# Optimization experiments

Measured on AMD Instinct MI355X. Metric: run time of the kernel, lower is better.

Reference implementation:

```python
import jax, jax.numpy as jnp
import numpy as np
from jax import lax


def _conv(x, w, padding):
    # NCHW input, OIHW weights, stride 1, no bias
    return lax.conv_general_dilated(x, w, (1, 1), padding,
                                    dimension_numbers=('NCHW', 'OIHW', 'NCHW'))


def setup_inputs() -> dict:
    key = jax.random.key(0)
    ks = jax.random.split(key, 6)
    B, C, H, W = 16, 512, 40, 40
    return {
        'exemplar': jax.random.normal(ks[0], (B, C, H, W), jnp.float32),
        'query':    jax.random.normal(ks[1], (B, C, H, W), jnp.float32),
        'w_e':  jax.random.normal(ks[2], (256, C, 1, 1), jnp.float32) * 0.01,
        'w_q':  jax.random.normal(ks[3], (256, C, 1, 1), jnp.float32) * 0.01,
        'w_c1': jax.random.normal(ks[4], (C, C, 3, 3), jnp.float32) * 0.01,
        'w_c2': jax.random.normal(ks[5], (C, C, 3, 3), jnp.float32) * 0.01,
    }


def reference(exemplar, query, w_e, w_q, w_c1, w_c2):
    B, C, H, W = query.shape
    N = H * W
    # 1x1 projections to 256-dim correlation space
    q_corr = _conv(query, w_q, 'VALID').reshape(B, -1, N)     # [B,256,N]
    e_corr = _conv(exemplar, w_e, 'VALID').reshape(B, -1, N)  # [B,256,N]
    # A[b, n_exemplar, m_query] = <e_corr[:, n], q_corr[:, m]>
    A = jnp.einsum('bcn,bcm->bnm', e_corr, q_corr)            # [B,N,N]
    # A1 = softmax over exemplar axis, then transpose (torch: softmax(A,dim=1).T)
    A1 = jnp.swapaxes(jax.nn.softmax(A, axis=1), 1, 2)        # [B,N,N]
    # Bm = softmax(A^T, dim=1).T  == softmax(A, axis=2)
    Bm = jnp.swapaxes(jax.nn.softmax(jnp.swapaxes(A, 1, 2), axis=1), 1, 2)
    e_flat = exemplar.reshape(B, C, N)
    q_flat = query.reshape(B, C, N)
    query_att = jnp.matmul(e_flat, A1)   # [B,C,N]
    exemplar_att = jnp.matmul(q_flat, Bm)  # [B,C,N]
    input1_att = _conv(exemplar_att.reshape(B, C, H, W), w_c1, 'SAME')
    input2_att = _conv(query_att.reshape(B, C, H, W), w_c2, 'SAME')
    return jnp.concatenate([input1_att, input2_att], axis=1)  # [B,2C,H,W]
```

## Files before the change

### kernel.cpp

```cpp
#include <hip/hip_runtime.h>

typedef unsigned short u16;
typedef __attribute__((ext_vector_type(8))) short bf16x8;
typedef __attribute__((ext_vector_type(4))) float f32x4;

__device__ __forceinline__ u16 f2bf(float f) {
  union { float f; unsigned u; } v; v.f = f;
  unsigned u = v.u;
  u += 0x7fffu + ((u >> 16) & 1u);
  return (u16)(u >> 16);
}

__device__ __forceinline__ void gll16(const void* g, void* l) {
  __builtin_amdgcn_global_load_lds(
      (const __attribute__((address_space(1))) void*)g,
      (__attribute__((address_space(3))) void*)l, 16, 0, 0);
}

__global__ __launch_bounds__(256) void transp_cast_x2(const float* __restrict__ ex,
                                                      const float* __restrict__ qu,
                                                      u16* __restrict__ xte,
                                                      u16* __restrict__ xtq) {
  __shared__ float t[32][33];
  int z = blockIdx.z;
  int b = z & 15;
  const float* xb = (z < 16 ? ex : qu) + (size_t)b * 819200;
  u16* xtb = (z < 16 ? xte : xtq) + (size_t)b * 819200;
  int n0 = blockIdx.x * 32, c0 = blockIdx.y * 32;
  int tx = threadIdx.x & 31, ty = threadIdx.x >> 5;
#pragma unroll
  for (int k = 0; k < 4; k++) {
    int c = ty + k * 8;
    t[c][tx] = xb[(size_t)(c0 + c) * 1600 + n0 + tx];
  }
  __syncthreads();
#pragma unroll
  for (int k = 0; k < 4; k++) {
    int n = ty + k * 8;
    xtb[(size_t)(n0 + n) * 512 + c0 + tx] = f2bf(t[tx][n]);
  }
}

__global__ void cast_w(const float* __restrict__ we, const float* __restrict__ wq,
                       u16* __restrict__ oe, u16* __restrict__ oq) {
  int i = blockIdx.x * 256 + threadIdx.x;
  oe[i] = f2bf(we[i]);
  oq[i] = f2bf(wq[i]);
}

__global__ void repack_wc(const float* __restrict__ w1, const float* __restrict__ w2,
                          u16* __restrict__ o1, u16* __restrict__ o2) {
  const float* w = blockIdx.y ? w2 : w1;
  u16* wr = blockIdx.y ? o2 : o1;
  int idx = blockIdx.x * 256 + threadIdx.x;
  int o = idx / 4608;
  int r = idx - o * 4608;
  int t = r >> 9;
  int c = r & 511;
  wr[idx] = f2bf(w[o * 4608 + c * 9 + t]);
}

__global__ void zero_mem(uint4* __restrict__ p, long n) {
  long i = (long)blockIdx.x * blockDim.x + threadIdx.x;
  long stride = (long)gridDim.x * blockDim.x;
  uint4 z; z.x = 0; z.y = 0; z.z = 0; z.w = 0;
  for (; i < n; i += stride) p[i] = z;
}

template <int MODE>
__global__ __launch_bounds__(256) void gemm_bt64(
    const u16* __restrict__ A, const u16* __restrict__ B, u16* __restrict__ C,
    const u16* __restrict__ A2, const u16* __restrict__ B2, u16* __restrict__ C2,
    int M, int N, int K, long sA, long sB, long sC) {
  __shared__ u16 lds_a[128 * 64];
  __shared__ u16 lds_b[128 * 64];
  int tid = threadIdx.x;
  int z = blockIdx.z, b = z & 15;
  const u16* Ab = (z < 16 ? A : A2) + (size_t)b * sA;
  const u16* Bb = (z < 16 ? B : B2) + (size_t)b * sB;
  u16* Cb = (z < 16 ? C : C2) + (size_t)b * sC;
  int m0 = blockIdx.x * 128, n0 = blockIdx.y * 128;

  int rsub = tid >> 3;
  int gch = (tid & 7) ^ (rsub & 7);
  long Kb = (long)K * 2;
  const char* pa[4];
  const char* pb[4];
#pragma unroll
  for (int c = 0; c < 4; c++) {
    int ra = m0 + 32 * c + rsub; ra = ra < M ? ra : M - 1;
    int rb = n0 + 32 * c + rsub; rb = rb < N ? rb : N - 1;
    pa[c] = (const char*)Ab + (long)ra * Kb + gch * 16;
    pb[c] = (const char*)Bb + (long)rb * Kb + gch * 16;
  }

  const f32x4 fzero = {0.f, 0.f, 0.f, 0.f};
  f32x4 acc[4][4];
#pragma unroll
  for (int mi = 0; mi < 4; mi++)
#pragma unroll
    for (int ni = 0; ni < 4; ni++) acc[mi][ni] = fzero;

  int wid = tid >> 6, lane = tid & 63;
  int wm = wid & 1, wn = wid >> 1;
  int lrow = lane & 15, lquad = lane >> 4;
  int sl = lrow & 7;

  int ksteps = K >> 6;
  for (int ks = 0; ks < ksteps; ks++) {
#pragma unroll
    for (int c = 0; c < 4; c++) {
      gll16(pa[c], (char*)lds_a + c * 4096 + tid * 16);
      gll16(pb[c], (char*)lds_b + c * 4096 + tid * 16);
      pa[c] += 128; pb[c] += 128;
    }
    __syncthreads();
#pragma unroll
    for (int k2 = 0; k2 < 2; k2++) {
      int sel = ((k2 << 2) | lquad) ^ sl;
      bf16x8 bv[4];
#pragma unroll
      for (int ni = 0; ni < 4; ni++) {
        int rowb = wn * 64 + ni * 16 + lrow;
        bv[ni] = *(const bf16x8*)((const char*)lds_b + rowb * 128 + sel * 16);
      }
#pragma unroll
      for (int mi = 0; mi < 4; mi++) {
        int rowa = wm * 64 + mi * 16 + lrow;
        bf16x8 av = *(const bf16x8*)((const char*)lds_a + rowa * 128 + sel * 16);
#pragma unroll
        for (int ni = 0; ni < 4; ni++)
          acc[mi][ni] =
              __builtin_amdgcn_mfma_f32_16x16x32_bf16(av, bv[ni], acc[mi][ni], 0, 0, 0);
      }
    }
    __syncthreads();
  }

#pragma unroll
  for (int mi = 0; mi < 4; mi++) {
#pragma unroll
    for (int r = 0; r < 4; r++) {
      int i = m0 + wm * 64 + mi * 16 + lquad * 4 + r;
      if (i >= M) continue;
#pragma unroll
      for (int ni = 0; ni < 4; ni++) {
        int j = n0 + wn * 64 + ni * 16 + lrow;
        if (j >= N) continue;
        float v = acc[mi][ni][r];
        if (MODE == 2) {
          int y = i / 40, x = i - y * 40;
          Cb[(size_t)((y + 1) * 42 + (x + 1)) * 512 + j] = f2bf(v);
        } else {
          Cb[(size_t)i * N + j] = f2bf(v);
        }
      }
    }
  }
}

__global__ __launch_bounds__(256) void gemm_corr_exp(
    const u16* __restrict__ A, const u16* __restrict__ B, u16* __restrict__ E,
    u16* __restrict__ ET, float* __restrict__ Zrow, float* __restrict__ Zcol) {
  __shared__ u16 lds_a[128 * 64];
  __shared__ u16 lds_b[128 * 64];
  int tid = threadIdx.x;
  int b = blockIdx.z;
  const u16* Ab = A + (size_t)b * 409600;
  const u16* Bb = B + (size_t)b * 409600;
  u16* Eb = E + (size_t)b * 2560000;
  u16* ETb = ET + (size_t)b * 2560000;
  int m0 = blockIdx.x * 128, n0 = blockIdx.y * 128;

  int rsub = tid >> 3;
  int gch = (tid & 7) ^ (rsub & 7);
  const char* pa[4];
  const char* pb[4];
#pragma unroll
  for (int c = 0; c < 4; c++) {
    int ra = m0 + 32 * c + rsub; ra = ra < 1600 ? ra : 1599;
    int rb = n0 + 32 * c + rsub; rb = rb < 1600 ? rb : 1599;
    pa[c] = (const char*)(Ab + (size_t)ra * 256) + gch * 16;
    pb[c] = (const char*)(Bb + (size_t)rb * 256) + gch * 16;
  }

  const f32x4 fzero = {0.f, 0.f, 0.f, 0.f};
  f32x4 acc[4][4];
#pragma unroll
  for (int mi = 0; mi < 4; mi++)
#pragma unroll
    for (int ni = 0; ni < 4; ni++) acc[mi][ni] = fzero;

  int wid = tid >> 6, lane = tid & 63;
  int wm = wid & 1, wn = wid >> 1;
  int lrow = lane & 15, lquad = lane >> 4;
  int sl = lrow & 7;

  for (int ks = 0; ks < 4; ks++) {
#pragma unroll
    for (int c = 0; c < 4; c++) {
      gll16(pa[c], (char*)lds_a + c * 4096 + tid * 16);
      gll16(pb[c], (char*)lds_b + c * 4096 + tid * 16);
      pa[c] += 128; pb[c] += 128;
    }
    __syncthreads();
#pragma unroll
    for (int k2 = 0; k2 < 2; k2++) {
      int sel = ((k2 << 2) | lquad) ^ sl;
      bf16x8 bv[4];
#pragma unroll
      for (int ni = 0; ni < 4; ni++) {
        int rowb = wn * 64 + ni * 16 + lrow;
        bv[ni] = *(const bf16x8*)((const char*)lds_b + rowb * 128 + sel * 16);
      }
#pragma unroll
      for (int mi = 0; mi < 4; mi++) {
        int rowa = wm * 64 + mi * 16 + lrow;
        bf16x8 av = *(const bf16x8*)((const char*)lds_a + rowa * 128 + sel * 16);
#pragma unroll
        for (int ni = 0; ni < 4; ni++)
          acc[mi][ni] =
              __builtin_amdgcn_mfma_f32_16x16x32_bf16(av, bv[ni], acc[mi][ni], 0, 0, 0);
      }
    }
    __syncthreads();
  }

  const int TS = 136;
  u16* T = lds_a;
  float colacc[4] = {0.f, 0.f, 0.f, 0.f};
#pragma unroll
  for (int s = 0; s < 4; s++) {
    if (wm == (s >> 1)) {
      int smi0 = (s & 1) * 2;
#pragma unroll
      for (int mi2 = 0; mi2 < 2; mi2++) {
        int mi = smi0 + mi2;
        float rowp[4] = {0.f, 0.f, 0.f, 0.f};
#pragma unroll
        for (int ni = 0; ni < 4; ni++) {
          int j = n0 + wn * 64 + ni * 16 + lrow;
          bool jv = j < 1600;
#pragma unroll
          for (int r = 0; r < 4; r++) {
            int i = m0 + wm * 64 + mi * 16 + lquad * 4 + r;
            float e = __expf(acc[mi][ni][r]);
            T[(mi2 * 16 + lquad * 4 + r) * TS + wn * 64 + ni * 16 + lrow] = f2bf(e);
            rowp[r] += jv ? e : 0.f;
            colacc[ni] += (i < 1600) ? e : 0.f;
          }
        }
#pragma unroll
        for (int r = 0; r < 4; r++) {
          float v = rowp[r];
          v += __shfl_xor(v, 1);
          v += __shfl_xor(v, 2);
          v += __shfl_xor(v, 4);
          v += __shfl_xor(v, 8);
          int i = m0 + wm * 64 + mi * 16 + lquad * 4 + r;
          if (lrow == 0 && i < 1600) atomicAdd(&Zrow[b * 1600 + i], v);
        }
      }
    }
    __syncthreads();
#pragma unroll
    for (int p = 0; p < 2; p++) {
      int jj = tid + p * 256;
      int ml = jj >> 4, n8 = jj & 15;
      int gi = m0 + s * 32 + ml, gj = n0 + n8 * 8;
      if (gi < 1600 && gj < 1600)
        *(uint4*)(Eb + (size_t)gi * 1600 + gj) = *(const uint4*)&T[ml * TS + n8 * 8];
    }
#pragma unroll
    for (int p = 0; p < 4; p++) {
      int jj = tid + p * 256;
      int n = jj >> 3, m4 = jj & 7;
      int gm = m0 + s * 32 + m4 * 4, gn = n0 + n;
      if (gn < 1600 && gm < 1600) {
        ushort4 v;
        v.x = T[(m4 * 4 + 0) * TS + n];
        v.y = T[(m4 * 4 + 1) * TS + n];
        v.z = T[(m4 * 4 + 2) * TS + n];
        v.w = T[(m4 * 4 + 3) * TS + n];
        *(ushort4*)(ETb + (size_t)gn * 1600 + gm) = v;
      }
    }
    __syncthreads();
  }
#pragma unroll
  for (int ni = 0; ni < 4; ni++) {
    float v = colacc[ni];
    v += __shfl_xor(v, 16);
    v += __shfl_xor(v, 32);
    int j = n0 + wn * 64 + ni * 16 + lrow;
    if (lquad == 0 && j < 1600) atomicAdd(&Zcol[b * 1600 + j], v);
  }
}

__global__ void scale_div(const float* __restrict__ ex, const float* __restrict__ qu,
                          const float* __restrict__ Zcol, const float* __restrict__ Zrow,
                          u16* __restrict__ ebf, u16* __restrict__ qbf) {
  const float* x; const float* Z; u16* o;
  if (blockIdx.y == 0) { x = ex; Z = Zcol; o = ebf; }
  else { x = qu; Z = Zrow; o = qbf; }
  size_t idx = (size_t)blockIdx.x * 256 + threadIdx.x;
  int b = (int)(idx / 819200);
  int i = (int)(idx % 1600);
  o[idx] = f2bf(x[idx] / Z[b * 1600 + i]);
}

__global__ __launch_bounds__(512, 2) void conv_gemm8p(
    const u16* __restrict__ W1, const u16* __restrict__ ATT1,
    const u16* __restrict__ W2, const u16* __restrict__ ATT2,
    float* __restrict__ out) {
  __shared__ u16 ldsA[32768];
  __shared__ u16 ldsB[32768];
  int tid = threadIdx.x;
  int z = blockIdx.z, b = z & 15, sel2 = z >> 4;
  const u16* W = sel2 ? W2 : W1;
  const u16* attb = (sel2 ? ATT2 : ATT1) + (size_t)b * 903168;
  float* outb = out + (size_t)b * 1638400 + (size_t)(sel2 ? 512 : 0) * 1600;
  int p0 = blockIdx.x * 256, o0 = blockIdx.y * 256;

  int rl = tid >> 2;
  int cs = (tid & 3) ^ ((rl >> 1) & 3);
  const char* pA0 = (const char*)(W + (size_t)(o0 + rl) * 4608) + cs * 16;
  const char* pA1 = pA0 + 128 * 9216;
  int pp0 = p0 + rl; pp0 = pp0 < 1600 ? pp0 : 1599;
  int y0 = pp0 / 40, x0 = pp0 - y0 * 40;
  const char* pB0 = (const char*)(attb + (size_t)(y0 * 42 + x0) * 512) + cs * 16;
  int pp1 = p0 + 128 + rl; pp1 = pp1 < 1600 ? pp1 : 1599;
  int y1 = pp1 / 40, x1 = pp1 - y1 * 40;
  const char* pB1 = (const char*)(attb + (size_t)(y1 * 42 + x1) * 512) + cs * 16;

  char* ldsAb = (char*)ldsA;
  char* ldsBb = (char*)ldsB;
  int dstT = tid * 16;

#define STAGE_A(d, kh, kt)                                              \
  {                                                                     \
    int ko = (kt) * 128 + (kh) * 64;                                    \
    gll16(pA0 + ko, ldsAb + ((d) * 2 + (kh)) * 16384 + dstT);           \
    gll16(pA1 + ko, ldsAb + ((d) * 2 + (kh)) * 16384 + 8192 + dstT);    \
  }
#define STAGE_B(d, kh, kt)                                              \
  {                                                                     \
    int tp = (kt) >> 3;                                                 \
    int ty = (tp * 11) >> 5;                                            \
    int tx = tp - ty * 3;                                               \
    int ko = (ty * 42 + tx) * 1024 + ((kt) & 7) * 128 + (kh) * 64;      \
    gll16(pB0 + ko, ldsBb + ((d) * 2 + (kh)) * 16384 + dstT);           \
    gll16(pB1 + ko, ldsBb + ((d) * 2 + (kh)) * 16384 + 8192 + dstT);    \
  }

  int wid = tid >> 6, lane = tid & 63;
  int wm = wid & 1, wn = wid >> 1;
  int lrow = lane & 15, lquad = lane >> 4;
  int csel = (lquad ^ ((lrow >> 1) & 3)) << 4;
  int aBase = (wm * 128 + lrow) * 64 + csel;
  int bBase = (wn * 64 + lrow) * 64 + csel;

  const f32x4 fzero = {0.f, 0.f, 0.f, 0.f};
  f32x4 acc[8][4];
#pragma unroll
  for (int mi = 0; mi < 8; mi++)
#pragma unroll
    for (int ni = 0; ni < 4; ni++) acc[mi][ni] = fzero;

  STAGE_B(0, 0, 0); STAGE_A(0, 0, 0); STAGE_B(0, 1, 0); STAGE_A(0, 1, 0);
  STAGE_B(1, 0, 1); STAGE_A(1, 0, 1); STAGE_B(1, 1, 1);
  asm volatile("s_waitcnt vmcnt(6)" ::: "memory");
  __builtin_amdgcn_s_barrier();

  bf16x8 bv0, bv1, bv2, bv3;

#define MFMA4(mi, av)                                                          \
  acc[mi][0] = __builtin_amdgcn_mfma_f32_16x16x32_bf16(av, bv0, acc[mi][0], 0, 0, 0); \
  acc[mi][1] = __builtin_amdgcn_mfma_f32_16x16x32_bf16(av, bv1, acc[mi][1], 0, 0, 0); \
  acc[mi][2] = __builtin_amdgcn_mfma_f32_16x16x32_bf16(av, bv2, acc[mi][2], 0, 0, 0); \
  acc[mi][3] = __builtin_amdgcn_mfma_f32_16x16x32_bf16(av, bv3, acc[mi][3], 0, 0, 0);

#define PHASE(d, kh, mh, STG, VM)                                              \
  {                                                                            \
    const char* ra_ = ldsAb + ((d) * 2 + (kh)) * 16384 + aBase + (mh) * 4096;  \
    bf16x8 av0 = *(const bf16x8*)(ra_);                                        \
    bf16x8 av1 = *(const bf16x8*)(ra_ + 1024);                                 \
    bf16x8 av2 = *(const bf16x8*)(ra_ + 2048);                                 \
    bf16x8 av3 = *(const bf16x8*)(ra_ + 3072);                                 \
    if ((mh) == 0) {                                                           \
      const char* rb_ = ldsBb + ((d) * 2 + (kh)) * 16384 + bBase;              \
      bv0 = *(const bf16x8*)(rb_);                                             \
      bv1 = *(const bf16x8*)(rb_ + 1024);                                      \
      bv2 = *(const bf16x8*)(rb_ + 2048);                                      \
      bv3 = *(const bf16x8*)(rb_ + 3072);                                      \
    }                                                                          \
    STG;                                                                       \
    VM;                                                                        \
    __builtin_amdgcn_s_barrier();                                              \
    asm volatile("s_waitcnt lgkmcnt(0)" ::: "memory");                         \
    __builtin_amdgcn_sched_barrier(0);                                         \
    __builtin_amdgcn_s_setprio(1);                                             \
    MFMA4((mh) * 4 + 0, av0);                                                  \
    MFMA4((mh) * 4 + 1, av1);                                                  \
    MFMA4((mh) * 4 + 2, av2);                                                  \
    MFMA4((mh) * 4 + 3, av3);                                                  \
    __builtin_amdgcn_s_setprio(0);                                             \
    __builtin_amdgcn_sched_barrier(0);                                         \
    __builtin_amdgcn_s_barrier();                                              \
  }

#define VMW asm volatile("s_waitcnt vmcnt(6)" ::: "memory")

#pragma unroll 1
  for (int it = 0; it < 36; ++it) {
    int ktb = it * 2;
    int kt1 = ktb + 1;
    int kt2 = ktb + 2 < 72 ? ktb + 2 : 71;
    int kt3 = ktb + 3 < 72 ? ktb + 3 : 71;
    PHASE(0, 0, 0, STAGE_A(1, 1, kt1), (void)0);
    PHASE(0, 0, 1, STAGE_B(0, 0, kt2), (void)0);
    PHASE(0, 1, 0, STAGE_A(0, 0, kt2), (void)0);
    PHASE(0, 1, 1, STAGE_B(0, 1, kt2), VMW);
    PHASE(1, 0, 0, STAGE_A(0, 1, kt2), (void)0);
    PHASE(1, 0, 1, STAGE_B(1, 0, kt3), (void)0);
    PHASE(1, 1, 0, STAGE_A(1, 0, kt3), (void)0);
    PHASE(1, 1, 1, STAGE_B(1, 1, kt3), VMW);
  }

#undef PHASE
#undef MFMA4
#undef VMW
#undef STAGE_A
#undef STAGE_B

#pragma unroll
  for (int mi = 0; mi < 8; mi++) {
#pragma unroll
    for (int r = 0; r < 4; r++) {
      int o = o0 + wm * 128 + mi * 16 + lquad * 4 + r;
      float* orow = outb + (size_t)o * 1600;
#pragma unroll
      for (int ni = 0; ni < 4; ni++) {
        int p = p0 + wn * 64 + ni * 16 + lrow;
        if (p < 1600) orow[p] = acc[mi][ni][r];
      }
    }
  }
}

extern "C" void kernel_launch(void* const* d_in, const int* in_sizes, int n_in,
                              void* d_out, int out_size, void* d_ws, size_t ws_size,
                              hipStream_t stream) {
  const float* ex = (const float*)d_in[0];
  const float* qu = (const float*)d_in[1];
  const float* w_e = (const float*)d_in[2];
  const float* w_q = (const float*)d_in[3];
  const float* w_c1 = (const float*)d_in[4];
  const float* w_c2 = (const float*)d_in[5];
  float* out = (float*)d_out;
  char* ws = (char*)d_ws;

  u16* E     = (u16*)(ws + 0L);
  u16* ET    = (u16*)(ws + 81920000L);
  u16* xt_e  = (u16*)(ws + 163840000L);
  u16* xt_q  = (u16*)(ws + 190054400L);
  u16* ecorr = (u16*)(ws + 216268800L);
  u16* qcorr = (u16*)(ws + 229376000L);
  u16* att_e = (u16*)(ws + 242483200L);
  u16* att_q = (u16*)(ws + 271384576L);
  float* Zrow = (float*)(ws + 300285952L);
  float* Zcol = (float*)(ws + 300388352L);
  u16* w_ebf = (u16*)(ws + 300490752L);
  u16* w_qbf = (u16*)(ws + 300752896L);
  u16* wr1   = (u16*)(ws + 301015040L);
  u16* wr2   = (u16*)(ws + 305733632L);

  transp_cast_x2<<<dim3(50, 16, 32), 256, 0, stream>>>(ex, qu, xt_e, xt_q);
  cast_w<<<dim3(512), 256, 0, stream>>>(w_e, w_q, w_ebf, w_qbf);
  repack_wc<<<dim3(9216, 2), 256, 0, stream>>>(w_c1, w_c2, wr1, wr2);
  zero_mem<<<dim3(2048), 256, 0, stream>>>((uint4*)att_e, 3625472L);

  gemm_bt64<0><<<dim3(13, 2, 32), 256, 0, stream>>>(
      xt_e, w_ebf, ecorr, xt_q, w_qbf, qcorr, 1600, 256, 512, 819200L, 0L, 409600L);

  gemm_corr_exp<<<dim3(13, 13, 16), 256, 0, stream>>>(ecorr, qcorr, E, ET, Zrow, Zcol);

  u16* ebf = xt_e;
  u16* qbf = xt_q;
  scale_div<<<dim3(51200, 2), 256, 0, stream>>>(ex, qu, Zcol, Zrow, ebf, qbf);

  gemm_bt64<2><<<dim3(13, 4, 32), 256, 0, stream>>>(
      E, ebf, att_q, ET, qbf, att_e, 1600, 512, 1600, 2560000L, 819200L, 903168L);

  conv_gemm8p<<<dim3(7, 2, 32), 512, 0, stream>>>(wr1, att_e, wr2, att_q, out);
}
```

Before: 867.0 us.

## Retile 3x3 conv GEMM to 256x224 tiles with 4x2 warp grid

Changes the conv GEMM output tile from 256x256 to 256x224 pixels, which grows the grid from 7 to 8 blocks along the pixel dimension. Each wave now computes a 64x112 sub-tile (4x7 MFMA fragments) instead of 128x64, under a 4x2 wave layout. The pipeline is restructured from eight half-phases per iteration to four full phases, each staging both A and B and waiting at vmcnt(8). The aim is to fill more CU slots and cut barrier count. The B staging still loads 256 rows, so some loads fetch unused data.

```diff
diff --git a/kernel.cpp b/kernel.cpp
--- a/kernel.cpp
+++ b/kernel.cpp
@@ -309,7 +309,7 @@
   o[idx] = f2bf(x[idx] / Z[b * 1600 + i]);
 }
 
-__global__ __launch_bounds__(512, 2) void conv_gemm8p(
+__global__ __launch_bounds__(512, 2) void conv_gemm4p(
     const u16* __restrict__ W1, const u16* __restrict__ ATT1,
     const u16* __restrict__ W2, const u16* __restrict__ ATT2,
     float* __restrict__ out) {
@@ -320,7 +320,7 @@
   const u16* W = sel2 ? W2 : W1;
   const u16* attb = (sel2 ? ATT2 : ATT1) + (size_t)b * 903168;
   float* outb = out + (size_t)b * 1638400 + (size_t)(sel2 ? 512 : 0) * 1600;
-  int p0 = blockIdx.x * 256, o0 = blockIdx.y * 256;
+  int p0 = blockIdx.x * 224, o0 = blockIdx.y * 256;
 
   int rl = tid >> 2;
   int cs = (tid & 3) ^ ((rl >> 1) & 3);
@@ -352,64 +352,66 @@
     gll16(pB0 + ko, ldsBb + ((d) * 2 + (kh)) * 16384 + dstT);           \
     gll16(pB1 + ko, ldsBb + ((d) * 2 + (kh)) * 16384 + 8192 + dstT);    \
   }
+#define STAGE_U(d, kh, kt) { STAGE_A(d, kh, kt); STAGE_B(d, kh, kt); }
 
   int wid = tid >> 6, lane = tid & 63;
-  int wm = wid & 1, wn = wid >> 1;
+  int wm = wid & 3, wn = wid >> 2;
   int lrow = lane & 15, lquad = lane >> 4;
   int csel = (lquad ^ ((lrow >> 1) & 3)) << 4;
-  int aBase = (wm * 128 + lrow) * 64 + csel;
-  int bBase = (wn * 64 + lrow) * 64 + csel;
+  int aBase = (wm * 64 + lrow) * 64 + csel;
+  int bBase = (wn * 112 + lrow) * 64 + csel;
 
   const f32x4 fzero = {0.f, 0.f, 0.f, 0.f};
-  f32x4 acc[8][4];
-#pragma unroll
-  for (int mi = 0; mi < 8; mi++)
-#pragma unroll
-    for (int ni = 0; ni < 4; ni++) acc[mi][ni] = fzero;
-
-  STAGE_B(0, 0, 0); STAGE_A(0, 0, 0); STAGE_B(0, 1, 0); STAGE_A(0, 1, 0);
-  STAGE_B(1, 0, 1); STAGE_A(1, 0, 1); STAGE_B(1, 1, 1);
-  asm volatile("s_waitcnt vmcnt(6)" ::: "memory");
+  f32x4 acc[4][7];
+#pragma unroll
+  for (int mi = 0; mi < 4; mi++)
+#pragma unroll
+    for (int ni = 0; ni < 7; ni++) acc[mi][ni] = fzero;
+
+  STAGE_U(0, 0, 0);
+  STAGE_U(0, 1, 0);
+  STAGE_U(1, 0, 1);
+  asm volatile("s_waitcnt vmcnt(8)" ::: "memory");
   __builtin_amdgcn_s_barrier();
 
-  bf16x8 bv0, bv1, bv2, bv3;
-
-#define MFMA4(mi, av)                                                          \
-  acc[mi][0] = __builtin_amdgcn_mfma_f32_16x16x32_bf16(av, bv0, acc[mi][0], 0, 0, 0); \
-  acc[mi][1] = __builtin_amdgcn_mfma_f32_16x16x32_bf16(av, bv1, acc[mi][1], 0, 0, 0); \
-  acc[mi][2] = __builtin_amdgcn_mfma_f32_16x16x32_bf16(av, bv2, acc[mi][2], 0, 0, 0); \
-  acc[mi][3] = __builtin_amdgcn_mfma_f32_16x16x32_bf16(av, bv3, acc[mi][3], 0, 0, 0);
-
-#define PHASE(d, kh, mh, STG, VM)                                              \
+#define MROW(mi, av)                                                                   \
+  acc[mi][0] = __builtin_amdgcn_mfma_f32_16x16x32_bf16(av, bv0, acc[mi][0], 0, 0, 0);  \
+  acc[mi][1] = __builtin_amdgcn_mfma_f32_16x16x32_bf16(av, bv1, acc[mi][1], 0, 0, 0);  \
+  acc[mi][2] = __builtin_amdgcn_mfma_f32_16x16x32_bf16(av, bv2, acc[mi][2], 0, 0, 0);  \
+  acc[mi][3] = __builtin_amdgcn_mfma_f32_16x16x32_bf16(av, bv3, acc[mi][3], 0, 0, 0);  \
+  acc[mi][4] = __builtin_amdgcn_mfma_f32_16x16x32_bf16(av, bv4, acc[mi][4], 0, 0, 0);  \
+  acc[mi][5] = __builtin_amdgcn_mfma_f32_16x16x32_bf16(av, bv5, acc[mi][5], 0, 0, 0);  \
+  acc[mi][6] = __builtin_amdgcn_mfma_f32_16x16x32_bf16(av, bv6, acc[mi][6], 0, 0, 0);
+
+#define PHASE(d, kh, STG)                                                      \
   {                                                                            \
-    const char* ra_ = ldsAb + ((d) * 2 + (kh)) * 16384 + aBase + (mh) * 4096;  \
+    const char* ra_ = ldsAb + ((d) * 2 + (kh)) * 16384 + aBase;                \
+    const char* rb_ = ldsBb + ((d) * 2 + (kh)) * 16384 + bBase;                \
     bf16x8 av0 = *(const bf16x8*)(ra_);                                        \
     bf16x8 av1 = *(const bf16x8*)(ra_ + 1024);                                 \
     bf16x8 av2 = *(const bf16x8*)(ra_ + 2048);                                 \
     bf16x8 av3 = *(const bf16x8*)(ra_ + 3072);                                 \
-    if ((mh) == 0) {                                                           \
-      const char* rb_ = ldsBb + ((d) * 2 + (kh)) * 16384 + bBase;              \
-      bv0 = *(const bf16x8*)(rb_);                                             \
-      bv1 = *(const bf16x8*)(rb_ + 1024);                                      \
-      bv2 = *(const bf16x8*)(rb_ + 2048);                                      \
-      bv3 = *(const bf16x8*)(rb_ + 3072);                                      \
-    }                                                                          \
+    bf16x8 bv0 = *(const bf16x8*)(rb_);                                        \
+    bf16x8 bv1 = *(const bf16x8*)(rb_ + 1024);                                 \
+    bf16x8 bv2 = *(const bf16x8*)(rb_ + 2048);                                 \
+    bf16x8 bv3 = *(const bf16x8*)(rb_ + 3072);                                 \
+    bf16x8 bv4 = *(const bf16x8*)(rb_ + 4096);                                 \
+    bf16x8 bv5 = *(const bf16x8*)(rb_ + 5120);                                 \
+    bf16x8 bv6 = *(const bf16x8*)(rb_ + 6144);                                 \
     STG;                                                                       \
-    VM;                                                                        \
+    asm volatile("s_waitcnt vmcnt(8)" ::: "memory");                           \
     __builtin_amdgcn_s_barrier();                                              \
     asm volatile("s_waitcnt lgkmcnt(0)" ::: "memory");                         \
     __builtin_amdgcn_sched_barrier(0);                                         \
     __builtin_amdgcn_s_setprio(1);                                             \
-    MFMA4((mh) * 4 + 0, av0);                                                  \
-    MFMA4((mh) * 4 + 1, av1);                                                  \
-    MFMA4((mh) * 4 + 2, av2);                                                  \
-    MFMA4((mh) * 4 + 3, av3);                                                  \
+    MROW(0, av0)                                                               \
+    MROW(1, av1)                                                               \
+    MROW(2, av2)                                                               \
+    MROW(3, av3)                                                               \
     __builtin_amdgcn_s_setprio(0);                                             \
     __builtin_amdgcn_sched_barrier(0);                                         \
     __builtin_amdgcn_s_barrier();                                              \
   }
-
-#define VMW asm volatile("s_waitcnt vmcnt(6)" ::: "memory")
 
 #pragma unroll 1
   for (int it = 0; it < 36; ++it) {
@@ -417,31 +419,27 @@
     int kt1 = ktb + 1;
     int kt2 = ktb + 2 < 72 ? ktb + 2 : 71;
     int kt3 = ktb + 3 < 72 ? ktb + 3 : 71;
-    PHASE(0, 0, 0, STAGE_A(1, 1, kt1), (void)0);
-    PHASE(0, 0, 1, STAGE_B(0, 0, kt2), (void)0);
-    PHASE(0, 1, 0, STAGE_A(0, 0, kt2), (void)0);
-    PHASE(0, 1, 1, STAGE_B(0, 1, kt2), VMW);
-    PHASE(1, 0, 0, STAGE_A(0, 1, kt2), (void)0);
-    PHASE(1, 0, 1, STAGE_B(1, 0, kt3), (void)0);
-    PHASE(1, 1, 0, STAGE_A(1, 0, kt3), (void)0);
-    PHASE(1, 1, 1, STAGE_B(1, 1, kt3), VMW);
+    PHASE(0, 0, STAGE_U(1, 1, kt1));
+    PHASE(0, 1, STAGE_U(0, 0, kt2));
+    PHASE(1, 0, STAGE_U(0, 1, kt2));
+    PHASE(1, 1, STAGE_U(1, 0, kt3));
   }
 
 #undef PHASE
-#undef MFMA4
-#undef VMW
+#undef MROW
+#undef STAGE_U
 #undef STAGE_A
 #undef STAGE_B
 
 #pragma unroll
-  for (int mi = 0; mi < 8; mi++) {
+  for (int mi = 0; mi < 4; mi++) {
 #pragma unroll
     for (int r = 0; r < 4; r++) {
-      int o = o0 + wm * 128 + mi * 16 + lquad * 4 + r;
+      int o = o0 + wm * 64 + mi * 16 + lquad * 4 + r;
       float* orow = outb + (size_t)o * 1600;
 #pragma unroll
-      for (int ni = 0; ni < 4; ni++) {
-        int p = p0 + wn * 64 + ni * 16 + lrow;
+      for (int ni = 0; ni < 7; ni++) {
+        int p = p0 + wn * 112 + ni * 16 + lrow;
         if (p < 1600) orow[p] = acc[mi][ni][r];
       }
     }
@@ -492,5 +490,5 @@
   gemm_bt64<2><<<dim3(13, 4, 32), 256, 0, stream>>>(
       E, ebf, att_q, ET, qbf, att_e, 1600, 512, 1600, 2560000L, 819200L, 903168L);
 
-  conv_gemm8p<<<dim3(7, 2, 32), 512, 0, stream>>>(wr1, att_e, wr2, att_q, out);
-}
+  conv_gemm4p<<<dim3(8, 2, 32), 512, 0, stream>>>(wr1, att_e, wr2, att_q, out);
+}
```

New measurement: 838.0 us. -3.3%, faster.
